# Kernel tuning notes

Hardware: AMD Instinct MI355X
Metric: run time of the kernel (lower is better)

The kernel has to match this reference:

```python
import jax, jax.numpy as jnp
import numpy as np

N = 8192
F_IN = 256
F_OUT = 64
ALPHA = 0.2  # LeakyReLU negative slope
MASK_VAL = -9e15


def setup_inputs() -> dict:
    key = jax.random.key(0)
    k1, k2, k3, k4 = jax.random.split(key, 4)
    h = jax.random.normal(k1, (N, F_IN), dtype=jnp.float32)
    adj = jax.random.randint(k2, (N, N), 0, 2, dtype=jnp.int32)  # 0/1 dense adjacency
    # Parameters (original creates them inside forward with xavier init; here fixed inputs)
    W = jax.random.normal(k3, (F_IN, F_OUT), dtype=jnp.float32) * (1.414 * np.sqrt(2.0 / (F_IN + F_OUT)))
    a = jax.random.normal(k4, (2 * F_OUT, 1), dtype=jnp.float32) * (1.414 * np.sqrt(2.0 / (2 * F_OUT + 1)))
    return {"h": h, "adj": adj, "W": W, "a": a}


def reference(h, adj, W, a):
    # Wh: [N, F_OUT]
    Wh = h @ W
    # e_ij = LeakyReLU(a^T [Wh_i ; Wh_j]) computed via broadcast instead of the
    f_src = Wh @ a[:F_OUT, 0]   # [N] contribution of row node i
    f_dst = Wh @ a[F_OUT:, 0]   # [N] contribution of col node j
    e = jax.nn.leaky_relu(f_src[:, None] + f_dst[None, :], negative_slope=ALPHA)  # [N, N]
    # adj-masked row softmax
    scores = jnp.where(adj > 0, e, MASK_VAL)
    attention = jax.nn.softmax(scores, axis=1)
    # dropout omitted (deterministic eval reference)
    h_prime = attention @ Wh  # [N, F_OUT]
    return jax.nn.elu(h_prime)  # concat=True branch
```

## Files before the change

kernel.cpp:

```cpp
#include <hip/hip_runtime.h>
#include <hip/hip_bf16.h>

#define NN 8192
#define FIN 256
#define FOUT 64
#define L2E 1.4426950408889634f
#define PADK 40

typedef __attribute__((ext_vector_type(8))) short short8;
typedef __attribute__((ext_vector_type(4))) float f32x4;
typedef __attribute__((ext_vector_type(4))) int   iv4;

#define BAR() do { \
  __asm__ __volatile__("s_waitcnt lgkmcnt(0)" ::: "memory"); \
  __builtin_amdgcn_s_barrier(); \
  __asm__ __volatile__("" ::: "memory"); \
} while (0)

__device__ __forceinline__ unsigned short f2bf(float x){
  unsigned u = __float_as_uint(x);
  u += 0x7FFFu + ((u >> 16) & 1u);
  return (unsigned short)(u >> 16);
}

__global__ __launch_bounds__(256) void k_pm(const float* __restrict__ h,
    const float* __restrict__ W, const float* __restrict__ a,
    unsigned short* __restrict__ WhT, float* __restrict__ fs,
    float* __restrict__ fd, unsigned* __restrict__ gmax_u){
  const int t = threadIdx.x;
  const int l = t & 63, wv = t >> 6;
  __shared__ float Ws[128*64];
  __shared__ float hs[8][128];
  const int rb = blockIdx.x * 8;
  float acc0 = 0.f, acc1 = 0.f;
  for (int half = 0; half < 2; ++half){
    if (half) __syncthreads();
    for (int i = t; i < 2048; i += 256)
      ((float4*)Ws)[i] = ((const float4*)W)[half*2048 + i];
    {
      int rr = t >> 5, cc = t & 31;
      ((float4*)&hs[rr][0])[cc] =
          *(const float4*)(h + (size_t)(rb+rr)*FIN + half*128 + cc*4);
    }
    __syncthreads();
    #pragma unroll 8
    for (int k = 0; k < 128; ++k){
      float wval = Ws[k*64 + l];
      acc0 = fmaf(hs[wv*2+0][k], wval, acc0);
      acc1 = fmaf(hs[wv*2+1][k], wval, acc1);
    }
  }
  const int r0 = rb + wv*2, r1 = r0 + 1;
  float a1 = a[l], a2 = a[64 + l];
  float p0 = acc0*a1, q0 = acc0*a2, p1 = acc1*a1, q1 = acc1*a2;
  #pragma unroll
  for (int m = 1; m < 64; m <<= 1){
    p0 += __shfl_xor(p0, m); q0 += __shfl_xor(q0, m);
    p1 += __shfl_xor(p1, m); q1 += __shfl_xor(q1, m);
  }
  if (l == 0){
    fs[r0] = p0*L2E; fs[r1] = p1*L2E; fd[r0] = q0*L2E; fd[r1] = q1*L2E;
    atomicMax(gmax_u, __float_as_uint(q0*L2E + 64.0f));
    atomicMax(gmax_u, __float_as_uint(q1*L2E + 64.0f));
  }
  WhT[(size_t)l*NN + r0] = f2bf(acc0);
  WhT[(size_t)l*NN + r1] = f2bf(acc1);
}

__device__ __forceinline__ void attn_math(iv4 da, iv4 db, f32x4 fv0, f32x4 fv1,
    short8 w0, short8 w1, short8 w2, short8 w3,
    float fsrL, float mL, f32x4* acc, float& s0, float& s1){
  const float fv[8] = {fv0[0],fv0[1],fv0[2],fv0[3], fv1[0],fv1[1],fv1[2],fv1[3]};
  const int   dv[8] = {da.x,da.y,da.z,da.w, db.x,db.y,db.z,db.w};
  float w[8];
  #pragma unroll
  for (int j = 0; j < 8; ++j){
    float x  = fsrL + fv[j];
    float tt = fmaxf(x, 0.2f*x);
    float e  = __builtin_amdgcn_exp2f(tt - mL);
    w[j] = dv[j] ? e : 0.0f;
  }
  s0 += (w[0]+w[2]) + (w[4]+w[6]);
  s1 += (w[1]+w[3]) + (w[5]+w[7]);
  short8 af;
  __hip_bfloat162* afp = (__hip_bfloat162*)&af;
  #pragma unroll
  for (int j = 0; j < 4; ++j)
    afp[j] = __float22bfloat162_rn(make_float2(w[2*j], w[2*j+1]));
  acc[0] = __builtin_amdgcn_mfma_f32_16x16x32_bf16(af, w0, acc[0], 0,0,0);
  acc[1] = __builtin_amdgcn_mfma_f32_16x16x32_bf16(af, w1, acc[1], 0,0,0);
  acc[2] = __builtin_amdgcn_mfma_f32_16x16x32_bf16(af, w2, acc[2], 0,0,0);
  acc[3] = __builtin_amdgcn_mfma_f32_16x16x32_bf16(af, w3, acc[3], 0,0,0);
}

__global__ __launch_bounds__(256, 4) void k_attn(const int* __restrict__ adj,
    const unsigned short* __restrict__ WhT, const float* __restrict__ fs,
    const float* __restrict__ fd, const unsigned* __restrict__ gmax_u,
    float* __restrict__ acc_out, float* __restrict__ s_out){
  __shared__ unsigned short bslab[2][64*PADK];
  __shared__ float fslab[2][32];
  const int t = threadIdx.x, l = t & 63, wv = t >> 6;
  const int g = blockIdx.x & 127;
  const int kchunk = blockIdx.x >> 7;
  const int row = l & 15, quad = l >> 4;
  const int ibase = g*64 + wv*16;
  const int irow  = ibase + row;
  const float gmaxL = __uint_as_float(*gmax_u) - 64.0f;
  const float fsrL  = fs[irow];
  const float xL    = fsrL + gmaxL;
  const float mL    = fmaxf(xL, 0.2f*xL);

  const unsigned jbase = (unsigned)kchunk*1024u;
  const unsigned sg_off = (unsigned)l*8192u + jbase + (unsigned)wv*8u;
  const int      sl_off = l*PADK + wv*8;
  const int      qsh    = quad*8;

  const iv4* __restrict__ ap =
      (const iv4*)(adj + (size_t)irow*8192u + jbase + (unsigned)qsh);

  f32x4 acc[4];
  #pragma unroll
  for (int nb = 0; nb < 4; ++nb) acc[nb] = (f32x4){0.f,0.f,0.f,0.f};

  {
    short8 v = *(const short8*)(WhT + sg_off);
    *(short8*)&bslab[0][sl_off] = v;
    if (t < 32) fslab[0][t] = fd[jbase + t];
  }
  iv4 c0a = ap[0], c0b = ap[1];
  iv4 c1a = ap[8], c1b = ap[9];

  float s0 = 0.f, s1 = 0.f;
  short8 nw; float nf = 0.f;

  #pragma unroll 1
  for (int s = 0; s < 32; s += 2){
    BAR();
    nw = *(const short8*)(WhT + sg_off + (s+1)*32);
    if (t < 32) nf = fd[jbase + (s+1)*32 + t];
    {
      f32x4 fv0 = *(const f32x4*)&fslab[0][qsh];
      f32x4 fv1 = *(const f32x4*)&fslab[0][qsh + 4];
      short8 w0 = *(const short8*)&bslab[0][( 0 + row)*PADK + qsh];
      short8 w1 = *(const short8*)&bslab[0][(16 + row)*PADK + qsh];
      short8 w2 = *(const short8*)&bslab[0][(32 + row)*PADK + qsh];
      short8 w3 = *(const short8*)&bslab[0][(48 + row)*PADK + qsh];
      attn_math(c0a, c0b, fv0, fv1, w0, w1, w2, w3, fsrL, mL, acc, s0, s1);
    }
    if (s + 2 < 32){ c0a = ap[(s+2)*8]; c0b = ap[(s+2)*8 + 1]; }
    *(short8*)&bslab[1][sl_off] = nw;
    if (t < 32) fslab[1][t] = nf;

    BAR();
    if (s + 2 < 32){
      nw = *(const short8*)(WhT + sg_off + (s+2)*32);
      if (t < 32) nf = fd[jbase + (s+2)*32 + t];
    }
    {
      f32x4 fv0 = *(const f32x4*)&fslab[1][qsh];
      f32x4 fv1 = *(const f32x4*)&fslab[1][qsh + 4];
      short8 w0 = *(const short8*)&bslab[1][( 0 + row)*PADK + qsh];
      short8 w1 = *(const short8*)&bslab[1][(16 + row)*PADK + qsh];
      short8 w2 = *(const short8*)&bslab[1][(32 + row)*PADK + qsh];
      short8 w3 = *(const short8*)&bslab[1][(48 + row)*PADK + qsh];
      attn_math(c1a, c1b, fv0, fv1, w0, w1, w2, w3, fsrL, mL, acc, s0, s1);
    }
    if (s + 3 < 32){ c1a = ap[(s+3)*8]; c1b = ap[(s+3)*8 + 1]; }
    if (s + 2 < 32){
      *(short8*)&bslab[0][sl_off] = nw;
      if (t < 32) fslab[0][t] = nf;
    }
  }

  float sacc = s0 + s1;
  sacc += __shfl_xor(sacc, 16);
  sacc += __shfl_xor(sacc, 32);
  if (l < 16) s_out[kchunk*NN + ibase + l] = sacc;
  float* op = acc_out + ((size_t)kchunk*NN + ibase)*FOUT;
  #pragma unroll
  for (int nb = 0; nb < 4; ++nb)
    #pragma unroll
    for (int r = 0; r < 4; ++r)
      op[(quad*4 + r)*FOUT + nb*16 + row] = acc[nb][r];
}

__global__ __launch_bounds__(256) void k_out(const float* __restrict__ acc,
    const float* __restrict__ s, float* __restrict__ out){
  const int idx = blockIdx.x*256 + threadIdx.x;
  const int i = idx >> 6;
  float num = 0.f, den = 0.f;
  #pragma unroll
  for (int ks = 0; ks < 8; ++ks){
    num += acc[idx + (size_t)ks*(NN*FOUT)];
    den += s[i + ks*NN];
  }
  float x = num / den;
  out[idx] = (x > 0.f) ? x : (__expf(x) - 1.0f);
}

extern "C" void kernel_launch(void* const* d_in, const int* in_sizes, int n_in,
                              void* d_out, int out_size, void* d_ws, size_t ws_size,
                              hipStream_t stream){
  const float* h   = (const float*)d_in[0];
  const int*   adj = (const int*)d_in[1];
  const float* W   = (const float*)d_in[2];
  const float* a   = (const float*)d_in[3];
  char* ws = (char*)d_ws;
  unsigned short* WhT = (unsigned short*)ws;
  float*    fs     = (float*)(ws + (1u<<20));
  float*    fd     = (float*)(ws + (1u<<20) + 32768);
  unsigned* gmax_u = (unsigned*)(ws + (1u<<20) + 65536);
  float*    acc    = (float*)(ws + (2u<<20));
  float*    s_ws   = (float*)(ws + (20u<<20));

  (void)hipMemsetAsync(gmax_u, 0, 4, stream);
  k_pm<<<1024, 256, 0, stream>>>(h, W, a, WhT, fs, fd, gmax_u);
  k_attn<<<1024, 256, 0, stream>>>(adj, WhT, fs, fd, gmax_u, acc, s_ws);
  k_out<<<2048, 256, 0, stream>>>(acc, s_ws, (float*)d_out);
}
```

Baseline: 516.9 us.

## Load adjacency coalesced per row and compress to ballot bitmasks, drop LDS staging

The attention kernel now reads each adjacency row with all 64 lanes contiguously (one row per load across 16 rows), converts the int entries into 64-bit ballot masks, and gives each lane its mask bits by shifting. WhT and fd tiles are loaded straight from global memory into registers with one-step prefetch, replacing the double-buffered LDS slabs and barriers. The aim is better coalescing on the dominant adjacency stream and no synchronisation cost. In exchange it needs more registers, so launch bounds drop to 2 blocks per SM, and every lane issues its own redundant WhT loads.

```diff
diff --git a/kernel.cpp b/kernel.cpp
--- a/kernel.cpp
+++ b/kernel.cpp
@@ -5,17 +5,11 @@
 #define FIN 256
 #define FOUT 64
 #define L2E 1.4426950408889634f
-#define PADK 40
 
 typedef __attribute__((ext_vector_type(8))) short short8;
 typedef __attribute__((ext_vector_type(4))) float f32x4;
 typedef __attribute__((ext_vector_type(4))) int   iv4;
-
-#define BAR() do { \
-  __asm__ __volatile__("s_waitcnt lgkmcnt(0)" ::: "memory"); \
-  __builtin_amdgcn_s_barrier(); \
-  __asm__ __volatile__("" ::: "memory"); \
-} while (0)
+typedef unsigned long long u64;
 
 __device__ __forceinline__ unsigned short f2bf(float x){
   unsigned u = __float_as_uint(x);
@@ -67,18 +61,29 @@
   WhT[(size_t)l*NN + r1] = f2bf(acc1);
 }
 
-__device__ __forceinline__ void attn_math(iv4 da, iv4 db, f32x4 fv0, f32x4 fv1,
+__device__ __forceinline__ void balrow(iv4 P, int RR, int row,
+    u64& B0, u64& B1, u64& B2, u64& B3){
+  u64 b0 = __ballot(P.x != 0);
+  u64 b1 = __ballot(P.y != 0);
+  u64 b2 = __ballot(P.z != 0);
+  u64 b3 = __ballot(P.w != 0);
+  if (row == RR){ B0 = b0; B1 = b1; B2 = b2; B3 = b3; }
+}
+
+__device__ __forceinline__ void attn_math(unsigned g0, unsigned g1,
+    unsigned g2, unsigned g3, f32x4 fv0, f32x4 fv1,
     short8 w0, short8 w1, short8 w2, short8 w3,
     float fsrL, float mL, f32x4* acc, float& s0, float& s1){
   const float fv[8] = {fv0[0],fv0[1],fv0[2],fv0[3], fv1[0],fv1[1],fv1[2],fv1[3]};
-  const int   dv[8] = {da.x,da.y,da.z,da.w, db.x,db.y,db.z,db.w};
+  const unsigned gb[8] = {g0&1u, g1&1u, g2&1u, g3&1u,
+                          g0&2u, g1&2u, g2&2u, g3&2u};
   float w[8];
   #pragma unroll
   for (int j = 0; j < 8; ++j){
     float x  = fsrL + fv[j];
     float tt = fmaxf(x, 0.2f*x);
     float e  = __builtin_amdgcn_exp2f(tt - mL);
-    w[j] = dv[j] ? e : 0.0f;
+    w[j] = gb[j] ? e : 0.0f;
   }
   s0 += (w[0]+w[2]) + (w[4]+w[6]);
   s1 += (w[1]+w[3]) + (w[5]+w[7]);
@@ -93,12 +98,10 @@
   acc[3] = __builtin_amdgcn_mfma_f32_16x16x32_bf16(af, w3, acc[3], 0,0,0);
 }
 
-__global__ __launch_bounds__(256, 4) void k_attn(const int* __restrict__ adj,
+__global__ __launch_bounds__(256, 2) void k_attn(const int* __restrict__ adj,
     const unsigned short* __restrict__ WhT, const float* __restrict__ fs,
     const float* __restrict__ fd, const unsigned* __restrict__ gmax_u,
     float* __restrict__ acc_out, float* __restrict__ s_out){
-  __shared__ unsigned short bslab[2][64*PADK];
-  __shared__ float fslab[2][32];
   const int t = threadIdx.x, l = t & 63, wv = t >> 6;
   const int g = blockIdx.x & 127;
   const int kchunk = blockIdx.x >> 7;
@@ -109,66 +112,90 @@
   const float fsrL  = fs[irow];
   const float xL    = fsrL + gmaxL;
   const float mL    = fmaxf(xL, 0.2f*xL);
-
   const unsigned jbase = (unsigned)kchunk*1024u;
-  const unsigned sg_off = (unsigned)l*8192u + jbase + (unsigned)wv*8u;
-  const int      sl_off = l*PADK + wv*8;
-  const int      qsh    = quad*8;
-
-  const iv4* __restrict__ ap =
-      (const iv4*)(adj + (size_t)irow*8192u + jbase + (unsigned)qsh);
+
+  const iv4* __restrict__ aq =
+      (const iv4*)(adj + (size_t)ibase*8192u + jbase) + l;
+  const unsigned short* __restrict__ wp0 = WhT + (size_t)( 0+row)*NN + jbase + quad*8;
+  const unsigned short* __restrict__ wp1 = WhT + (size_t)(16+row)*NN + jbase + quad*8;
+  const unsigned short* __restrict__ wp2 = WhT + (size_t)(32+row)*NN + jbase + quad*8;
+  const unsigned short* __restrict__ wp3 = WhT + (size_t)(48+row)*NN + jbase + quad*8;
+  const float* __restrict__ fp = fd + jbase + quad*8;
 
   f32x4 acc[4];
   #pragma unroll
   for (int nb = 0; nb < 4; ++nb) acc[nb] = (f32x4){0.f,0.f,0.f,0.f};
 
-  {
-    short8 v = *(const short8*)(WhT + sg_off);
-    *(short8*)&bslab[0][sl_off] = v;
-    if (t < 32) fslab[0][t] = fd[jbase + t];
-  }
-  iv4 c0a = ap[0], c0b = ap[1];
-  iv4 c1a = ap[8], c1b = ap[9];
+  u64 Bc0=0,Bc1=0,Bc2=0,Bc3=0, Bn0=0,Bn1=0,Bn2=0,Bn3=0;
+  iv4 p0,p1,p2,p3,p4,p5,p6,p7;
+
+  p0 = aq[0*2048]; p1 = aq[1*2048]; p2 = aq[2*2048]; p3 = aq[3*2048];
+  p4 = aq[4*2048]; p5 = aq[5*2048]; p6 = aq[6*2048]; p7 = aq[7*2048];
+  balrow(p0,0,row,Bc0,Bc1,Bc2,Bc3); balrow(p1,1,row,Bc0,Bc1,Bc2,Bc3);
+  balrow(p2,2,row,Bc0,Bc1,Bc2,Bc3); balrow(p3,3,row,Bc0,Bc1,Bc2,Bc3);
+  balrow(p4,4,row,Bc0,Bc1,Bc2,Bc3); balrow(p5,5,row,Bc0,Bc1,Bc2,Bc3);
+  balrow(p6,6,row,Bc0,Bc1,Bc2,Bc3); balrow(p7,7,row,Bc0,Bc1,Bc2,Bc3);
+  p0 = aq[ 8*2048]; p1 = aq[ 9*2048]; p2 = aq[10*2048]; p3 = aq[11*2048];
+  p4 = aq[12*2048]; p5 = aq[13*2048]; p6 = aq[14*2048]; p7 = aq[15*2048];
+  balrow(p0, 8,row,Bc0,Bc1,Bc2,Bc3); balrow(p1, 9,row,Bc0,Bc1,Bc2,Bc3);
+  balrow(p2,10,row,Bc0,Bc1,Bc2,Bc3); balrow(p3,11,row,Bc0,Bc1,Bc2,Bc3);
+  balrow(p4,12,row,Bc0,Bc1,Bc2,Bc3); balrow(p5,13,row,Bc0,Bc1,Bc2,Bc3);
+  balrow(p6,14,row,Bc0,Bc1,Bc2,Bc3); balrow(p7,15,row,Bc0,Bc1,Bc2,Bc3);
+
+  short8 wA = *(const short8*)(wp0);
+  short8 wB = *(const short8*)(wp1);
+  short8 wC = *(const short8*)(wp2);
+  short8 wD = *(const short8*)(wp3);
+  f32x4 fva = *(const f32x4*)(fp);
+  f32x4 fvb = *(const f32x4*)(fp + 4);
 
   float s0 = 0.f, s1 = 0.f;
-  short8 nw; float nf = 0.f;
 
   #pragma unroll 1
-  for (int s = 0; s < 32; s += 2){
-    BAR();
-    nw = *(const short8*)(WhT + sg_off + (s+1)*32);
-    if (t < 32) nf = fd[jbase + (s+1)*32 + t];
-    {
-      f32x4 fv0 = *(const f32x4*)&fslab[0][qsh];
-      f32x4 fv1 = *(const f32x4*)&fslab[0][qsh + 4];
-      short8 w0 = *(const short8*)&bslab[0][( 0 + row)*PADK + qsh];
-      short8 w1 = *(const short8*)&bslab[0][(16 + row)*PADK + qsh];
-      short8 w2 = *(const short8*)&bslab[0][(32 + row)*PADK + qsh];
-      short8 w3 = *(const short8*)&bslab[0][(48 + row)*PADK + qsh];
-      attn_math(c0a, c0b, fv0, fv1, w0, w1, w2, w3, fsrL, mL, acc, s0, s1);
-    }
-    if (s + 2 < 32){ c0a = ap[(s+2)*8]; c0b = ap[(s+2)*8 + 1]; }
-    *(short8*)&bslab[1][sl_off] = nw;
-    if (t < 32) fslab[1][t] = nf;
-
-    BAR();
-    if (s + 2 < 32){
-      nw = *(const short8*)(WhT + sg_off + (s+2)*32);
-      if (t < 32) nf = fd[jbase + (s+2)*32 + t];
-    }
-    {
-      f32x4 fv0 = *(const f32x4*)&fslab[1][qsh];
-      f32x4 fv1 = *(const f32x4*)&fslab[1][qsh + 4];
-      short8 w0 = *(const short8*)&bslab[1][( 0 + row)*PADK + qsh];
-      short8 w1 = *(const short8*)&bslab[1][(16 + row)*PADK + qsh];
-      short8 w2 = *(const short8*)&bslab[1][(32 + row)*PADK + qsh];
-      short8 w3 = *(const short8*)&bslab[1][(48 + row)*PADK + qsh];
-      attn_math(c1a, c1b, fv0, fv1, w0, w1, w2, w3, fsrL, mL, acc, s0, s1);
-    }
-    if (s + 3 < 32){ c1a = ap[(s+3)*8]; c1b = ap[(s+3)*8 + 1]; }
-    if (s + 2 < 32){
-      *(short8*)&bslab[0][sl_off] = nw;
-      if (t < 32) fslab[0][t] = nf;
+  for (int h = 0; h < 4; ++h){
+    const iv4* __restrict__ aqn = aq + (h+1)*64;
+    #pragma unroll
+    for (int ss = 0; ss < 8; ++ss){
+      const int s = h*8 + ss;
+      short8 nwA = wA, nwB = wB, nwC = wC, nwD = wD;
+      f32x4 nfva = fva, nfvb = fvb;
+      if (h < 3 || ss < 7){
+        const int o = (s+1)*32;
+        nwA = *(const short8*)(wp0 + o);
+        nwB = *(const short8*)(wp1 + o);
+        nwC = *(const short8*)(wp2 + o);
+        nwD = *(const short8*)(wp3 + o);
+        nfva = *(const f32x4*)(fp + o);
+        nfvb = *(const f32x4*)(fp + o + 4);
+      }
+      if (h < 3){
+        if (ss == 0){ p0=aqn[0*2048]; p1=aqn[1*2048]; p2=aqn[ 2*2048]; p3=aqn[ 3*2048]; }
+        if (ss == 1){ p4=aqn[4*2048]; p5=aqn[5*2048]; p6=aqn[ 6*2048]; p7=aqn[ 7*2048]; }
+        if (ss == 4){ p0=aqn[8*2048]; p1=aqn[9*2048]; p2=aqn[10*2048]; p3=aqn[11*2048]; }
+        if (ss == 5){ p4=aqn[12*2048]; p5=aqn[13*2048]; p6=aqn[14*2048]; p7=aqn[15*2048]; }
+      }
+      {
+        const int sh = ss*8 + quad*2;
+        unsigned g0 = (unsigned)(Bc0 >> sh);
+        unsigned g1 = (unsigned)(Bc1 >> sh);
+        unsigned g2 = (unsigned)(Bc2 >> sh);
+        unsigned g3 = (unsigned)(Bc3 >> sh);
+        attn_math(g0,g1,g2,g3, fva,fvb, wA,wB,wC,wD, fsrL, mL, acc, s0, s1);
+      }
+      wA = nwA; wB = nwB; wC = nwC; wD = nwD; fva = nfva; fvb = nfvb;
+      if (h < 3 && ss == 3){
+        balrow(p0,0,row,Bn0,Bn1,Bn2,Bn3); balrow(p1,1,row,Bn0,Bn1,Bn2,Bn3);
+        balrow(p2,2,row,Bn0,Bn1,Bn2,Bn3); balrow(p3,3,row,Bn0,Bn1,Bn2,Bn3);
+        balrow(p4,4,row,Bn0,Bn1,Bn2,Bn3); balrow(p5,5,row,Bn0,Bn1,Bn2,Bn3);
+        balrow(p6,6,row,Bn0,Bn1,Bn2,Bn3); balrow(p7,7,row,Bn0,Bn1,Bn2,Bn3);
+      }
+      if (h < 3 && ss == 7){
+        balrow(p0, 8,row,Bn0,Bn1,Bn2,Bn3); balrow(p1, 9,row,Bn0,Bn1,Bn2,Bn3);
+        balrow(p2,10,row,Bn0,Bn1,Bn2,Bn3); balrow(p3,11,row,Bn0,Bn1,Bn2,Bn3);
+        balrow(p4,12,row,Bn0,Bn1,Bn2,Bn3); balrow(p5,13,row,Bn0,Bn1,Bn2,Bn3);
+        balrow(p6,14,row,Bn0,Bn1,Bn2,Bn3); balrow(p7,15,row,Bn0,Bn1,Bn2,Bn3);
+        Bc0 = Bn0; Bc1 = Bn1; Bc2 = Bn2; Bc3 = Bn3;
+      }
     }
   }
 
```

Measured after the change: 512.6 us. About the same (-0.8%).
